# Kernel optimization log

Measured on AMD Instinct MI355X. Metric: run time of the kernel, lower is better.

Reference implementation:

```python
import jax, jax.numpy as jnp
import numpy as np

B, G = 64, 48            # events, grid side -> N = B*G*G nodes
N = B * G * G
DIMS = [128, 102, 73, 44, 16]   # channel schedule from GraphZ defaults
KERN = 3                 # GMM kernels on the conv layer
MAXV = 1.0               # Cartesian(max_value=neighbors=1)


def _build_graph():
    # 3x3 window graph (radius 1, self loops) per event, as in window_edges
    ix, iy = np.meshgrid(np.arange(G), np.arange(G), indexing='ij')
    ix, iy = ix.ravel(), iy.ravel()
    srcs, tgts = [], []
    for dx in (-1, 0, 1):
        for dy in (-1, 0, 1):
            jx, jy = ix + dx, iy + dy
            m = (jx >= 0) & (jx < G) & (jy >= 0) & (jy < G)
            srcs.append(jx[m] * G + jy[m])
            tgts.append(ix[m] * G + iy[m])
    src, tgt = np.concatenate(srcs), np.concatenate(tgts)
    base = (np.arange(B) * G * G)[:, None]
    ei = np.stack([(base + src[None]).ravel(), (base + tgt[None]).ravel()])
    pos = np.stack([np.tile(ix, B).astype(np.float32),
                    np.tile(iy, B).astype(np.float32),
                    np.repeat(np.arange(B), G * G).astype(np.float32)], axis=1)
    return ei.astype(np.int32), pos


def setup_inputs() -> dict:
    key = jax.random.key(0)
    ks = jax.random.split(key, 16)
    ei, pos = _build_graph()
    inp = {
        'x': jax.random.normal(ks[0], (N, DIMS[0]), jnp.float32),
        'pos': jnp.asarray(pos),
        'edge_index': jnp.asarray(ei),
    }
    # pointwise layer 0: 128->102 (+BN)
    inp['w0'] = jax.random.normal(ks[1], (DIMS[0], DIMS[1]), jnp.float32) * (1.0 / np.sqrt(DIMS[0]))
    inp['b0'] = jnp.zeros((DIMS[1],), jnp.float32)
    inp['gamma0'] = jnp.ones((DIMS[1],), jnp.float32)
    inp['beta0'] = jnp.zeros((DIMS[1],), jnp.float32)
    # pointwise layer 1: 102->73 (+BN)
    inp['w1'] = jax.random.normal(ks[2], (DIMS[1], DIMS[2]), jnp.float32) * (1.0 / np.sqrt(DIMS[1]))
    inp['b1'] = jnp.zeros((DIMS[2],), jnp.float32)
    inp['gamma1'] = jnp.ones((DIMS[2],), jnp.float32)
    inp['beta1'] = jnp.zeros((DIMS[2],), jnp.float32)
    # GMM conv layer 2: 73->44, 3 gaussian kernels (+BN)
    inp['w2'] = jax.random.normal(ks[3], (DIMS[2], DIMS[3]), jnp.float32) * (1.0 / np.sqrt(DIMS[2]))
    inp['g2'] = jax.random.normal(ks[4], (DIMS[2], KERN * DIMS[3]), jnp.float32) * (1.0 / np.sqrt(DIMS[2]))
    inp['mu2'] = jax.random.uniform(ks[5], (KERN, 2), jnp.float32)
    inp['sigma2'] = jax.random.uniform(ks[6], (KERN, 2), jnp.float32) + 0.5
    inp['b2'] = jnp.zeros((DIMS[3],), jnp.float32)
    inp['gamma2'] = jnp.ones((DIMS[3],), jnp.float32)
    inp['beta2'] = jnp.zeros((DIMS[3],), jnp.float32)
    # pointwise layer 3: 44->16
    inp['w3'] = jax.random.normal(ks[7], (DIMS[3], DIMS[4]), jnp.float32) * (1.0 / np.sqrt(DIMS[3]))
    inp['b3'] = jnp.zeros((DIMS[4],), jnp.float32)
    return inp


def _bn(x, gamma, beta):
    # BatchNorm1d training forward: biased batch stats over the node dim
    m = jnp.mean(x, axis=0)
    v = jnp.mean((x - m) ** 2, axis=0)
    return (x - m) * jax.lax.rsqrt(v + 1e-5) * gamma + beta


def _gmm_conv(x, ei, ea, g, mu, sigma, w_root, b, n):
    # PyG GMMConv (separate_gaussians=False, aggr='mean', root_weight, bias)
    E = ea.shape[0]
    kk = mu.shape[0]
    out = w_root.shape[1]
    xj = (x @ g)[ei[0]].reshape(E, kk, out)                 # gather transformed src feats
    gauss = jnp.exp(jnp.sum(-0.5 * (ea[:, None, :] - mu[None]) ** 2
                            / (1e-15 + sigma[None] ** 2), axis=-1))  # [E, K]
    msg = jnp.einsum('eko,ek->eo', xj, gauss)               # [E, out]
    s = jax.ops.segment_sum(msg, ei[1], num_segments=n)     # scatter-add to targets
    c = jax.ops.segment_sum(jnp.ones((E,), x.dtype), ei[1], num_segments=n)
    return s / jnp.maximum(c, 1.0)[:, None] + x @ w_root + b


def reference(x, pos, edge_index, w0, b0, gamma0, beta0, w1, b1, gamma1, beta1,
              w2, g2, mu2, sigma2, b2, gamma2, beta2, w3, b3):
    n = x.shape[0]
    pos2 = pos[:, :2]
    # Cartesian(max_value=1, norm=True): pseudo coords in [0, 1]
    ea = (pos2[edge_index[0]] - pos2[edge_index[1]]) / (2.0 * MAXV) + 0.5
    # layers 0,1: knn_graph(k=0) -> empty edge set -> GMMConv = root Linear + bias
    h = _bn(x @ w0 + b0, gamma0, beta0)
    h = _bn(h @ w1 + b1, gamma1, beta1)
    # layer 2: window-edge GMMConv with 3 gaussian kernels
    h = _bn(_gmm_conv(h, edge_index, ea, g2, mu2, sigma2, w2, b2, n), gamma2, beta2)
    # layer 3: pointwise, no norm
    return h @ w3 + b3
```

## Files before the change

### kernel.cpp

```cpp
#include <hip/hip_runtime.h>

#define GRIDW 48
#define NNODES 147456
#define NTILES 2304
#define GB 512
#define NSH 8
#define SHS 128

typedef __attribute__((ext_vector_type(8))) short short8;
typedef __attribute__((ext_vector_type(4))) float f32x4;

__device__ inline unsigned short f2bf(float f) {
    union { float f; unsigned u; } v; v.f = f;
    unsigned r = v.u + 0x7FFFu + ((v.u >> 16) & 1u);
    return (unsigned short)(r >> 16);
}
__device__ inline float bf2f(unsigned short h) {
    union { unsigned u; float f; } v; v.u = ((unsigned)h) << 16;
    return v.f;
}

__global__ void prep(const float* __restrict__ w0, const float* __restrict__ b0,
                     const float* __restrict__ w1, const float* __restrict__ b1,
                     const float* __restrict__ g2, const float* __restrict__ w2,
                     const float* __restrict__ b2, const float* __restrict__ w3,
                     const float* __restrict__ b3,
                     unsigned short* __restrict__ wt0, unsigned short* __restrict__ wt1,
                     unsigned short* __restrict__ wt2, unsigned short* __restrict__ wt3,
                     float* __restrict__ biasf0, float* __restrict__ biasf1,
                     float* __restrict__ biasf2, float* __restrict__ biasf3,
                     float* __restrict__ statz) {
    int id = blockIdx.x * 256 + threadIdx.x;
    if (id < 14336) {
        int col = id >> 7, k = id & 127;
        wt0[id] = (col < 102) ? f2bf(w0[k * 102 + col]) : (unsigned short)0;
    } else if (id < 24576) {
        int e = id - 14336; int col = e >> 7, k = e & 127;
        wt1[e] = (col < 73 && k < 102) ? f2bf(w1[k * 73 + col]) : (unsigned short)0;
    } else if (id < 41472) {
        int e = id - 24576; int col = e / 96, k = e - (e / 96) * 96;
        unsigned short v = 0;
        if (k < 73) v = (col < 132) ? f2bf(g2[k * 132 + col]) : f2bf(w2[k * 44 + (col - 132)]);
        wt2[e] = v;
    } else if (id < 42496) {
        int e = id - 41472; int col = e >> 6, k = e & 63;
        wt3[e] = (k < 44) ? f2bf(w3[k * 16 + col]) : (unsigned short)0;
    } else if (id < 42608) { int c = id - 42496; biasf0[c] = (c < 102) ? b0[c] : 0.f; }
    else if (id < 42688) { int c = id - 42608; biasf1[c] = (c < 73) ? b1[c] : 0.f; }
    else if (id < 42864) { int c = id - 42688; biasf2[c] = (c < 132) ? 0.f : b2[c - 132]; }
    else if (id < 42880) { int c = id - 42864; biasf3[c] = b3[c]; }
    else if (id < 49024) { statz[id - 42880] = 0.f; }
}

template<int K, int KP, int MP, int MOUT, int PREVM, int BNSRC,
         bool STATS, bool OUTBF, bool ABF16>
__global__ __launch_bounds__(256) void gemm_p(
    const void* __restrict__ Ain, const unsigned short* __restrict__ WT,
    const float* __restrict__ biasf,
    const float* __restrict__ q0, const float* __restrict__ q1,
    const float* __restrict__ q2, const float* __restrict__ q3,
    float invN, void* __restrict__ Yout,
    float* __restrict__ sumO, float* __restrict__ ssO)
{
    constexpr int KS = KP + 8;
    constexpr int NCF = MP / 16;
    constexpr int UPR = ABF16 ? (K / 8) : (K / 4);
    constexpr int TOT = 64 * UPR;
    constexpr int NLD = (TOT + 255) / 256;
    __shared__ __align__(16) unsigned short As[2][64 * KS];
    __shared__ __align__(16) unsigned short Bs[MP * KS];
    __shared__ float bnA[KP], bnB[KP];

    const int tid = threadIdx.x;
    const int lane = tid & 63, wv = tid >> 6, qd = lane >> 4, lc = lane & 15;

    if (BNSRC == 1) {
        if (tid < KP) {
            float a = 0.f, b = 0.f;
            if (tid < PREVM) {
                float s0 = 0.f, s1 = 0.f;
#pragma unroll
                for (int sh = 0; sh < NSH; ++sh) {
                    s0 += q0[sh * SHS + tid];
                    s1 += q1[sh * SHS + tid];
                }
                float m = s0 * invN;
                float v = s1 * invN - m * m;
                float sc = q2[tid] * rsqrtf(v + 1e-5f);
                a = sc; b = q3[tid] - m * sc;
            }
            bnA[tid] = a; bnB[tid] = b;
        }
    }
    for (int g = tid; g < MP * (KP / 8); g += 256) {
        int col = g / (KP / 8), u = g - col * (KP / 8);
        *(uint4*)&Bs[col * KS + u * 8] = *(const uint4*)&WT[(size_t)col * KP + u * 8];
    }
    if constexpr (KP > K) {
        constexpr int PADU = (KP - K) / 2;
        for (int g = tid; g < 64 * PADU; g += 256) {
            int row = g / PADU, u = g - row * PADU;
            *(unsigned*)&As[0][row * KS + K + u * 2] = 0u;
            *(unsigned*)&As[1][row * KS + K + u * 2] = 0u;
        }
    }

    float bvr[NCF];
#pragma unroll
    for (int cf = 0; cf < NCF; ++cf) bvr[cf] = biasf[cf * 16 + lc];

    float cs[NCF], cq[NCF];
    if (STATS) {
#pragma unroll
        for (int cf = 0; cf < NCF; ++cf) { cs[cf] = 0.f; cq[cf] = 0.f; }
    }

    uint4 pfb[NLD];
    float4 pff[NLD];

    int t = blockIdx.x;
#pragma unroll
    for (int i = 0; i < NLD; ++i) {
        int g = tid + 256 * i;
        if (g < TOT) {
            if constexpr (ABF16)
                pfb[i] = *(const uint4*)((const unsigned short*)Ain + (size_t)t * 64 * K + g * 8);
            else
                pff[i] = *(const float4*)((const float*)Ain + (size_t)t * 64 * K + g * 4);
        }
    }
    __syncthreads();

    int buf = 0;
    for (; t < NTILES; t += GB) {
#pragma unroll
        for (int i = 0; i < NLD; ++i) {
            int g = tid + 256 * i;
            if (g < TOT) {
                int row = g / UPR, u = g - row * UPR;
                if constexpr (ABF16) {
                    uint4 w = pfb[i];
                    if (BNSRC != 0) {
                        unsigned* wp = (unsigned*)&w;
#pragma unroll
                        for (int pp = 0; pp < 4; ++pp) {
                            int kk = u * 8 + 2 * pp;
                            float lo = bf2f((unsigned short)(wp[pp] & 0xFFFFu)) * bnA[kk] + bnB[kk];
                            float hi = bf2f((unsigned short)(wp[pp] >> 16)) * bnA[kk + 1] + bnB[kk + 1];
                            wp[pp] = (unsigned)f2bf(lo) | ((unsigned)f2bf(hi) << 16);
                        }
                    }
                    *(uint4*)&As[buf][row * KS + u * 8] = w;
                } else {
                    float4 v = pff[i];
                    if (BNSRC != 0) {
                        int kk = u * 4;
                        v.x = v.x * bnA[kk] + bnB[kk];
                        v.y = v.y * bnA[kk + 1] + bnB[kk + 1];
                        v.z = v.z * bnA[kk + 2] + bnB[kk + 2];
                        v.w = v.w * bnA[kk + 3] + bnB[kk + 3];
                    }
                    unsigned lo = (unsigned)f2bf(v.x) | ((unsigned)f2bf(v.y) << 16);
                    unsigned hi = (unsigned)f2bf(v.z) | ((unsigned)f2bf(v.w) << 16);
                    *(uint2*)&As[buf][row * KS + u * 4] = make_uint2(lo, hi);
                }
            }
        }
        int t2 = t + GB;
        if (t2 < NTILES) {
#pragma unroll
            for (int i = 0; i < NLD; ++i) {
                int g = tid + 256 * i;
                if (g < TOT) {
                    if constexpr (ABF16)
                        pfb[i] = *(const uint4*)((const unsigned short*)Ain + (size_t)t2 * 64 * K + g * 8);
                    else
                        pff[i] = *(const float4*)((const float*)Ain + (size_t)t2 * 64 * K + g * 4);
                }
            }
        }
        __syncthreads();

        f32x4 acc[NCF];
#pragma unroll
        for (int cf = 0; cf < NCF; ++cf) acc[cf] = (f32x4){0.f, 0.f, 0.f, 0.f};
#pragma unroll
        for (int kt = 0; kt < KP / 32; ++kt) {
            const int kb = kt * 32 + qd * 8;
            short8 a = *(const short8*)&As[buf][(wv * 16 + lc) * KS + kb];
#pragma unroll
            for (int cf = 0; cf < NCF; ++cf) {
                short8 b = *(const short8*)&Bs[(cf * 16 + lc) * KS + kb];
                acc[cf] = __builtin_amdgcn_mfma_f32_16x16x32_bf16(a, b, acc[cf], 0, 0, 0);
            }
        }
#pragma unroll
        for (int cf = 0; cf < NCF; ++cf) {
            const int col = cf * 16 + lc;
            const float bv = bvr[cf];
#pragma unroll
            for (int rr = 0; rr < 4; ++rr) {
                float v = acc[cf][rr] + bv;
                int row = t * 64 + wv * 16 + qd * 4 + rr;
                if (OUTBF) ((unsigned short*)Yout)[(size_t)row * MP + col] = f2bf(v);
                else       ((float*)Yout)[(size_t)row * MP + col] = v;
                if (STATS) { cs[cf] += v; cq[cf] += v * v; }
            }
        }
        buf ^= 1;
    }

    if (STATS) {
        __syncthreads();
        float* red = (float*)As;
        float* redq = red + 4 * MP;
#pragma unroll
        for (int cf = 0; cf < NCF; ++cf) {
            float s = cs[cf], qq = cq[cf];
            s += __shfl_down(s, 32, 64); s += __shfl_down(s, 16, 64);
            qq += __shfl_down(qq, 32, 64); qq += __shfl_down(qq, 16, 64);
            if (lane < 16) {
                red[wv * MP + cf * 16 + lane] = s;
                redq[wv * MP + cf * 16 + lane] = qq;
            }
        }
        __syncthreads();
        if (tid < MOUT) {
            float s = red[tid] + red[MP + tid] + red[2 * MP + tid] + red[3 * MP + tid];
            float qq = redq[tid] + redq[MP + tid] + redq[2 * MP + tid] + redq[3 * MP + tid];
            const int sh = blockIdx.x & (NSH - 1);
            atomicAdd(&sumO[sh * SHS + tid], s);
            atomicAdd(&ssO[sh * SHS + tid], qq);
        }
    }
}

__device__ inline void load_u(const unsigned short* __restrict__ TR, int b,
                              int jx, int iy, int c0, const float (*gy)[3],
                              float* __restrict__ u) {
#pragma unroll
    for (int j = 0; j < 12; ++j) u[j] = 0.f;
    if (jx < 0 || jx >= GRIDW) return;
    const unsigned short* rowp = TR + (size_t)(b * 2304 + jx * 48) * 176;
#pragma unroll
    for (int dy = -1; dy <= 1; ++dy) {
        int jy = iy + dy;
        if (jy < 0 || jy >= GRIDW) continue;
        const unsigned short* np = rowp + (size_t)jy * 176 + c0;
#pragma unroll
        for (int k = 0; k < 3; ++k) {
            uint2 v = *(const uint2*)(np + k * 44);
            float g = gy[dy + 1][k];
            u[k * 4 + 0] += g * bf2f((unsigned short)(v.x & 0xFFFFu));
            u[k * 4 + 1] += g * bf2f((unsigned short)(v.x >> 16));
            u[k * 4 + 2] += g * bf2f((unsigned short)(v.y & 0xFFFFu));
            u[k * 4 + 3] += g * bf2f((unsigned short)(v.y >> 16));
        }
    }
}

__global__ __launch_bounds__(256) void gmm_stencil(
    const unsigned short* __restrict__ TR, unsigned short* __restrict__ C,
    const float* __restrict__ mu, const float* __restrict__ sigma,
    float* __restrict__ sum2, float* __restrict__ ss2)
{
    __shared__ float gx[3][3], gy[3][3];
    __shared__ float red[88];
    const int tid = threadIdx.x;
    if (tid < 88) red[tid] = 0.f;
    if (tid < 18) {
        int d = (tid / 3) % 3, k = tid % 3;
        bool isy = tid >= 9;
        float e = 0.5f * (float)(d - 1) + 0.5f;
        float mm = mu[k * 2 + (isy ? 1 : 0)];
        float sg = sigma[k * 2 + (isy ? 1 : 0)];
        float v = expf(-0.5f * (e - mm) * (e - mm) / (1e-15f + sg * sg));
        if (isy) gy[d][k] = v; else gx[d][k] = v;
    }
    __syncthreads();

    const int xcd = blockIdx.x & 7;
    const int bi  = blockIdx.x >> 3;
    const int b   = xcd * 8 + bi / 33;
    const unsigned tau = (unsigned)(bi % 33) * 256u + (unsigned)tid;
    const int og = (int)(tau % 11u);
    const unsigned r1 = tau / 11u;
    const int iy = (int)(r1 % 48u);
    const int x0 = (int)(r1 / 48u) * 3;
    const int c0 = og * 4;

    float u0[12], u1[12], u2[12];
    load_u(TR, b, x0 - 1, iy, c0, gy, u0);
    load_u(TR, b, x0,     iy, c0, gy, u1);
    float s4[4] = {0, 0, 0, 0}, q4[4] = {0, 0, 0, 0};
    int ny = 1 + (iy > 0) + (iy < GRIDW - 1);
#pragma unroll
    for (int st = 0; st < 3; ++st) {
        int ix = x0 + st;
        float* ua = (st == 0) ? u0 : ((st == 1) ? u1 : u2);
        float* ub = (st == 0) ? u1 : ((st == 1) ? u2 : u0);
        float* uc = (st == 0) ? u2 : ((st == 1) ? u0 : u1);
        load_u(TR, b, ix + 1, iy, c0, gy, uc);
        int nx = 1 + (ix > 0) + (ix < GRIDW - 1);
        float inv = 1.f / (float)(nx * ny);
        int node = b * 2304 + ix * 48 + iy;
        uint2 rv = *(const uint2*)(TR + (size_t)node * 176 + 132 + c0);
        float o[4];
#pragma unroll
        for (int j = 0; j < 4; ++j) {
            float acc = 0.f;
#pragma unroll
            for (int k = 0; k < 3; ++k)
                acc += gx[0][k] * ua[k * 4 + j] + gx[1][k] * ub[k * 4 + j]
                     + gx[2][k] * uc[k * 4 + j];
            o[j] = acc * inv;
        }
        o[0] += bf2f((unsigned short)(rv.x & 0xFFFFu));
        o[1] += bf2f((unsigned short)(rv.x >> 16));
        o[2] += bf2f((unsigned short)(rv.y & 0xFFFFu));
        o[3] += bf2f((unsigned short)(rv.y >> 16));
        unsigned lo = (unsigned)f2bf(o[0]) | ((unsigned)f2bf(o[1]) << 16);
        unsigned hi = (unsigned)f2bf(o[2]) | ((unsigned)f2bf(o[3]) << 16);
        *(uint2*)&C[(size_t)node * 48 + c0] = make_uint2(lo, hi);
        if (og == 10)
            *(uint2*)&C[(size_t)node * 48 + 44] = make_uint2(0u, 0u);
#pragma unroll
        for (int j = 0; j < 4; ++j) { s4[j] += o[j]; q4[j] += o[j] * o[j]; }
    }
#pragma unroll
    for (int j = 0; j < 4; ++j) {
        atomicAdd(&red[c0 + j], s4[j]);
        atomicAdd(&red[44 + c0 + j], q4[j]);
    }
    __syncthreads();
    if (tid < 88) {
        const int sh = blockIdx.x & (NSH - 1);
        if (tid < 44) atomicAdd(&sum2[sh * SHS + tid], red[tid]);
        else          atomicAdd(&ss2[sh * SHS + tid - 44], red[tid]);
    }
}

extern "C" void kernel_launch(void* const* d_in, const int* in_sizes, int n_in,
                              void* d_out, int out_size, void* d_ws, size_t ws_size,
                              hipStream_t stream) {
    const float* x      = (const float*)d_in[0];
    const float* w0     = (const float*)d_in[3];
    const float* b0     = (const float*)d_in[4];
    const float* gamma0 = (const float*)d_in[5];
    const float* beta0  = (const float*)d_in[6];
    const float* w1     = (const float*)d_in[7];
    const float* b1     = (const float*)d_in[8];
    const float* gamma1 = (const float*)d_in[9];
    const float* beta1  = (const float*)d_in[10];
    const float* w2     = (const float*)d_in[11];
    const float* g2     = (const float*)d_in[12];
    const float* mu2    = (const float*)d_in[13];
    const float* sigma2 = (const float*)d_in[14];
    const float* b2     = (const float*)d_in[15];
    const float* gamma2 = (const float*)d_in[16];
    const float* beta2  = (const float*)d_in[17];
    const float* w3     = (const float*)d_in[18];
    const float* b3     = (const float*)d_in[19];
    float* out = (float*)d_out;

    const int N = NNODES;
    const float invN = 1.0f / (float)N;

    const size_t tailOff = (size_t)N * 132;
    size_t need = (tailOff + 300000) * sizeof(float);
    if (ws_size < need) return;

    float* ws = (float*)d_ws;
    unsigned short* bufY1 = (unsigned short*)ws;
    unsigned short* bufC  = (unsigned short*)ws;
    unsigned short* bufY0 = (unsigned short*)(ws + (size_t)N * 44);
    unsigned short* bufTR = bufY0;

    float* tail = ws + tailOff;
    float* sum0 = tail;
    float* ss0  = tail + 1024;
    float* sum1 = tail + 2048;
    float* ss1  = tail + 3072;
    float* sum2 = tail + 4096;
    float* ss2  = tail + 5120;
    float* biasf0 = tail + 6144;
    float* biasf1 = tail + 6256;
    float* biasf2 = tail + 6336;
    float* biasf3 = tail + 6512;
    unsigned short* wt0 = (unsigned short*)(tail + 6528);
    unsigned short* wt1 = wt0 + 14336;
    unsigned short* wt2 = wt1 + 10240;
    unsigned short* wt3 = wt2 + 16896;

    prep<<<192, 256, 0, stream>>>(w0, b0, w1, b1, g2, w2, b2, w3, b3,
                                  wt0, wt1, wt2, wt3,
                                  biasf0, biasf1, biasf2, biasf3, tail);

    gemm_p<128, 128, 112, 102, 0, 0, true, true, false><<<GB, 256, 0, stream>>>(
        x, wt0, biasf0, nullptr, nullptr, nullptr, nullptr, invN, bufY0, sum0, ss0);

    gemm_p<112, 128, 80, 73, 102, 1, true, true, true><<<GB, 256, 0, stream>>>(
        bufY0, wt1, biasf1, sum0, ss0, gamma0, beta0, invN, bufY1, sum1, ss1);

    gemm_p<80, 96, 176, 176, 73, 1, false, true, true><<<GB, 256, 0, stream>>>(
        bufY1, wt2, biasf2, sum1, ss1, gamma1, beta1, invN, bufTR, nullptr, nullptr);

    gmm_stencil<<<2112, 256, 0, stream>>>(bufTR, bufC, mu2, sigma2, sum2, ss2);

    gemm_p<48, 64, 16, 16, 44, 1, false, false, true><<<GB, 256, 0, stream>>>(
        bufC, wt3, biasf3, sum2, ss2, gamma2, beta2, invN, out, nullptr, nullptr);
}
```

Measured before the change: 248.7 us.

## Stage three grid rows in LDS per block for GMM stencil

The GMM stencil now uses one block per (event, grid row) and cooperatively copies the three neighbouring rows of transformed features into shared memory, about 50 KB. All 3x3 neighbour reads are then served from LDS instead of repeated global loads, with boundary handling moved to multiplicative masks. The launch grows from 2112 to 3072 blocks and per-thread register rotation is replaced by a task loop. The cost is large LDS use per block, which limits occupancy, plus more shared atomics per output.

```diff
diff --git a/kernel.cpp b/kernel.cpp
--- a/kernel.cpp
+++ b/kernel.cpp
@@ -18,6 +18,14 @@
 __device__ inline float bf2f(unsigned short h) {
     union { unsigned u; float f; } v; v.u = ((unsigned)h) << 16;
     return v.f;
+}
+__device__ __forceinline__ f32x4 b2v(uint2 v) {
+    f32x4 r;
+    r.x = bf2f((unsigned short)(v.x & 0xFFFFu));
+    r.y = bf2f((unsigned short)(v.x >> 16));
+    r.z = bf2f((unsigned short)(v.y & 0xFFFFu));
+    r.w = bf2f((unsigned short)(v.y >> 16));
+    return r;
 }
 
 __global__ void prep(const float* __restrict__ w0, const float* __restrict__ b0,
@@ -235,36 +243,13 @@
     }
 }
 
-__device__ inline void load_u(const unsigned short* __restrict__ TR, int b,
-                              int jx, int iy, int c0, const float (*gy)[3],
-                              float* __restrict__ u) {
-#pragma unroll
-    for (int j = 0; j < 12; ++j) u[j] = 0.f;
-    if (jx < 0 || jx >= GRIDW) return;
-    const unsigned short* rowp = TR + (size_t)(b * 2304 + jx * 48) * 176;
-#pragma unroll
-    for (int dy = -1; dy <= 1; ++dy) {
-        int jy = iy + dy;
-        if (jy < 0 || jy >= GRIDW) continue;
-        const unsigned short* np = rowp + (size_t)jy * 176 + c0;
-#pragma unroll
-        for (int k = 0; k < 3; ++k) {
-            uint2 v = *(const uint2*)(np + k * 44);
-            float g = gy[dy + 1][k];
-            u[k * 4 + 0] += g * bf2f((unsigned short)(v.x & 0xFFFFu));
-            u[k * 4 + 1] += g * bf2f((unsigned short)(v.x >> 16));
-            u[k * 4 + 2] += g * bf2f((unsigned short)(v.y & 0xFFFFu));
-            u[k * 4 + 3] += g * bf2f((unsigned short)(v.y >> 16));
-        }
-    }
-}
-
 __global__ __launch_bounds__(256) void gmm_stencil(
     const unsigned short* __restrict__ TR, unsigned short* __restrict__ C,
     const float* __restrict__ mu, const float* __restrict__ sigma,
     float* __restrict__ sum2, float* __restrict__ ss2)
 {
-    __shared__ float gx[3][3], gy[3][3];
+    __shared__ __align__(16) unsigned short rows[3][8448];
+    __shared__ float gxs[3][3], gys[3][3];
     __shared__ float red[88];
     const int tid = threadIdx.x;
     if (tid < 88) red[tid] = 0.f;
@@ -275,66 +260,111 @@
         float mm = mu[k * 2 + (isy ? 1 : 0)];
         float sg = sigma[k * 2 + (isy ? 1 : 0)];
         float v = expf(-0.5f * (e - mm) * (e - mm) / (1e-15f + sg * sg));
-        if (isy) gy[d][k] = v; else gx[d][k] = v;
-    }
+        if (isy) gys[d][k] = v; else gxs[d][k] = v;
+    }
+
+    const int wg  = blockIdx.x;
+    const int xcd = wg & 7;
+    const int idx = wg >> 3;
+    const int gb  = xcd * 384 + idx;
+    const int b   = gb / 48;
+    const int ix  = gb - b * 48;
+
+    const int rA = (ix > 0) ? ix - 1 : 0;
+    const int rC = (ix < GRIDW - 1) ? ix + 1 : GRIDW - 1;
+    const unsigned short* s0 = TR + (size_t)(b * 2304 + rA * 48) * 176;
+    const unsigned short* s1 = TR + (size_t)(b * 2304 + ix * 48) * 176;
+    const unsigned short* s2 = TR + (size_t)(b * 2304 + rC * 48) * 176;
+    for (int e = tid; e < 1056; e += 256)
+        *(uint4*)&rows[0][e * 8] = *(const uint4*)(s0 + (size_t)e * 8);
+    for (int e = tid; e < 1056; e += 256)
+        *(uint4*)&rows[1][e * 8] = *(const uint4*)(s1 + (size_t)e * 8);
+    for (int e = tid; e < 1056; e += 256)
+        *(uint4*)&rows[2][e * 8] = *(const uint4*)(s2 + (size_t)e * 8);
     __syncthreads();
 
-    const int xcd = blockIdx.x & 7;
-    const int bi  = blockIdx.x >> 3;
-    const int b   = xcd * 8 + bi / 33;
-    const unsigned tau = (unsigned)(bi % 33) * 256u + (unsigned)tid;
-    const int og = (int)(tau % 11u);
-    const unsigned r1 = tau / 11u;
-    const int iy = (int)(r1 % 48u);
-    const int x0 = (int)(r1 / 48u) * 3;
-    const int c0 = og * 4;
-
-    float u0[12], u1[12], u2[12];
-    load_u(TR, b, x0 - 1, iy, c0, gy, u0);
-    load_u(TR, b, x0,     iy, c0, gy, u1);
-    float s4[4] = {0, 0, 0, 0}, q4[4] = {0, 0, 0, 0};
-    int ny = 1 + (iy > 0) + (iy < GRIDW - 1);
-#pragma unroll
-    for (int st = 0; st < 3; ++st) {
-        int ix = x0 + st;
-        float* ua = (st == 0) ? u0 : ((st == 1) ? u1 : u2);
-        float* ub = (st == 0) ? u1 : ((st == 1) ? u2 : u0);
-        float* uc = (st == 0) ? u2 : ((st == 1) ? u0 : u1);
-        load_u(TR, b, ix + 1, iy, c0, gy, uc);
-        int nx = 1 + (ix > 0) + (ix < GRIDW - 1);
-        float inv = 1.f / (float)(nx * ny);
-        int node = b * 2304 + ix * 48 + iy;
-        uint2 rv = *(const uint2*)(TR + (size_t)node * 176 + 132 + c0);
-        float o[4];
-#pragma unroll
-        for (int j = 0; j < 4; ++j) {
-            float acc = 0.f;
-#pragma unroll
-            for (int k = 0; k < 3; ++k)
-                acc += gx[0][k] * ua[k * 4 + j] + gx[1][k] * ub[k * 4 + j]
-                     + gx[2][k] * uc[k * 4 + j];
-            o[j] = acc * inv;
-        }
-        o[0] += bf2f((unsigned short)(rv.x & 0xFFFFu));
-        o[1] += bf2f((unsigned short)(rv.x >> 16));
-        o[2] += bf2f((unsigned short)(rv.y & 0xFFFFu));
-        o[3] += bf2f((unsigned short)(rv.y >> 16));
-        unsigned lo = (unsigned)f2bf(o[0]) | ((unsigned)f2bf(o[1]) << 16);
-        unsigned hi = (unsigned)f2bf(o[2]) | ((unsigned)f2bf(o[3]) << 16);
+    const float gx00 = gxs[0][0], gx01 = gxs[0][1], gx02 = gxs[0][2];
+    const float gx10 = gxs[1][0], gx11 = gxs[1][1], gx12 = gxs[1][2];
+    const float gx20 = gxs[2][0], gx21 = gxs[2][1], gx22 = gxs[2][2];
+    const float gy00 = gys[0][0], gy01 = gys[0][1], gy02 = gys[0][2];
+    const float gy10 = gys[1][0], gy11 = gys[1][1], gy12 = gys[1][2];
+    const float gy20 = gys[2][0], gy21 = gys[2][1], gy22 = gys[2][2];
+
+    const float wxm = (ix > 0) ? 1.f : 0.f;
+    const float wxp = (ix < GRIDW - 1) ? 1.f : 0.f;
+    const int nx = 1 + (ix > 0) + (ix < GRIDW - 1);
+
+    for (int task = tid; task < 528; task += 256) {
+        const int og = task % 11;
+        const int iy = task / 11;
+        const int c0 = og * 4;
+        const int iym = (iy > 0) ? iy - 1 : 0;
+        const int iyp = (iy < GRIDW - 1) ? iy + 1 : GRIDW - 1;
+        const float my0 = (iy > 0) ? 1.f : 0.f;
+        const float my2 = (iy < GRIDW - 1) ? 1.f : 0.f;
+        const int ny = 1 + (iy > 0) + (iy < GRIDW - 1);
+        const float inv = 1.f / (float)(nx * ny);
+
+        const int om = iym * 176 + c0;
+        const int o0 = iy  * 176 + c0;
+        const int op = iyp * 176 + c0;
+
+#define YC(U0, U1, U2, SLOT, WX)                                               \
+        f32x4 U0, U1, U2;                                                      \
+        {                                                                      \
+            const unsigned short* p_ = &rows[SLOT][0];                         \
+            uint2 m0 = *(const uint2*)(p_ + om);                               \
+            uint2 m1 = *(const uint2*)(p_ + om + 44);                          \
+            uint2 m2 = *(const uint2*)(p_ + om + 88);                          \
+            uint2 z0 = *(const uint2*)(p_ + o0);                               \
+            uint2 z1 = *(const uint2*)(p_ + o0 + 44);                          \
+            uint2 z2 = *(const uint2*)(p_ + o0 + 88);                          \
+            uint2 pp0 = *(const uint2*)(p_ + op);                              \
+            uint2 pp1 = *(const uint2*)(p_ + op + 44);                         \
+            uint2 pp2 = *(const uint2*)(p_ + op + 88);                         \
+            U0 = ((WX) * my0 * gy00) * b2v(m0);                                \
+            U0 += ((WX) * gy10) * b2v(z0);                                     \
+            U0 += ((WX) * my2 * gy20) * b2v(pp0);                              \
+            U1 = ((WX) * my0 * gy01) * b2v(m1);                                \
+            U1 += ((WX) * gy11) * b2v(z1);                                     \
+            U1 += ((WX) * my2 * gy21) * b2v(pp1);                              \
+            U2 = ((WX) * my0 * gy02) * b2v(m2);                                \
+            U2 += ((WX) * gy12) * b2v(z2);                                     \
+            U2 += ((WX) * my2 * gy22) * b2v(pp2);                              \
+        }
+
+        YC(uL0, uL1, uL2, 0, wxm)
+        YC(uC0, uC1, uC2, 1, 1.f)
+        YC(uR0, uR1, uR2, 2, wxp)
+#undef YC
+
+        uint2 rv = *(const uint2*)(&rows[1][o0 + 132]);
+        f32x4 o = (f32x4){0.f, 0.f, 0.f, 0.f};
+        o += gx00 * uL0 + gx10 * uC0 + gx20 * uR0;
+        o += gx01 * uL1 + gx11 * uC1 + gx21 * uR1;
+        o += gx02 * uL2 + gx12 * uC2 + gx22 * uR2;
+        o = o * inv;
+        o += b2v(rv);
+
+        const int node = b * 2304 + ix * 48 + iy;
+        unsigned lo = (unsigned)f2bf(o.x) | ((unsigned)f2bf(o.y) << 16);
+        unsigned hi = (unsigned)f2bf(o.z) | ((unsigned)f2bf(o.w) << 16);
         *(uint2*)&C[(size_t)node * 48 + c0] = make_uint2(lo, hi);
         if (og == 10)
             *(uint2*)&C[(size_t)node * 48 + 44] = make_uint2(0u, 0u);
-#pragma unroll
-        for (int j = 0; j < 4; ++j) { s4[j] += o[j]; q4[j] += o[j] * o[j]; }
-    }
-#pragma unroll
-    for (int j = 0; j < 4; ++j) {
-        atomicAdd(&red[c0 + j], s4[j]);
-        atomicAdd(&red[44 + c0 + j], q4[j]);
+
+        atomicAdd(&red[c0 + 0], o.x);
+        atomicAdd(&red[c0 + 1], o.y);
+        atomicAdd(&red[c0 + 2], o.z);
+        atomicAdd(&red[c0 + 3], o.w);
+        atomicAdd(&red[44 + c0 + 0], o.x * o.x);
+        atomicAdd(&red[44 + c0 + 1], o.y * o.y);
+        atomicAdd(&red[44 + c0 + 2], o.z * o.z);
+        atomicAdd(&red[44 + c0 + 3], o.w * o.w);
     }
     __syncthreads();
     if (tid < 88) {
-        const int sh = blockIdx.x & (NSH - 1);
+        const int sh = wg & (NSH - 1);
         if (tid < 44) atomicAdd(&sum2[sh * SHS + tid], red[tid]);
         else          atomicAdd(&ss2[sh * SHS + tid - 44], red[tid]);
     }
@@ -405,7 +435,7 @@
     gemm_p<80, 96, 176, 176, 73, 1, false, true, true><<<GB, 256, 0, stream>>>(
         bufY1, wt2, biasf2, sum1, ss1, gamma1, beta1, invN, bufTR, nullptr, nullptr);
 
-    gmm_stencil<<<2112, 256, 0, stream>>>(bufTR, bufC, mu2, sigma2, sum2, ss2);
+    gmm_stencil<<<3072, 256, 0, stream>>>(bufTR, bufC, mu2, sigma2, sum2, ss2);
 
     gemm_p<48, 64, 16, 16, 44, 1, false, false, true><<<GB, 256, 0, stream>>>(
         bufC, wt3, biasf3, sum2, ss2, gamma2, beta2, invN, out, nullptr, nullptr);
```

Result: slower. 292.3 us (+17.6%).
